# Kernel tuning notes

Hardware: AMD Instinct MI355X
Metric: run time of the kernel (lower is better)

Reference implementation:

```python
import jax, jax.numpy as jnp
import numpy as np

B = 65536
DIM = 8
HIS_LEN = 5
KIND_LEN = 10
HIS_ITEM_DIM = (1 + KIND_LEN) * DIM  # 88
ALL_DIM = DIM * (5 + KIND_LEN) + HIS_ITEM_DIM  # 208


def _linear_params(key, in_dim, out_dim):
    k1, k2 = jax.random.split(key)
    bound = 1.0 / np.sqrt(in_dim)
    w = jax.random.uniform(k1, (out_dim, in_dim), jnp.float32, -bound, bound)
    b = jax.random.uniform(k2, (out_dim,), jnp.float32, -bound, bound)
    return w, b


def setup_inputs() -> dict:
    key = jax.random.key(0)
    ks = jax.random.split(key, 20)
    inp = {
        'userid': jax.random.randint(ks[0], (B, 1), 0, 1000000),
        'itemid': jax.random.randint(ks[1], (B, 1), 0, 1000000),
        'user_age': jax.random.randint(ks[2], (B, 1), 0, 8),
        'gender': jax.random.randint(ks[3], (B, 1), 0, 3),
        'user_occupation': jax.random.randint(ks[4], (B, 1), 0, 25),
        'item_kind': jax.random.randint(ks[5], (B, KIND_LEN), 0, 20),
        'item_id_his': jax.random.randint(ks[6], (B, HIS_LEN), 0, 1000000),
        'item_kind_his': jax.random.randint(ks[7], (B, HIS_LEN, KIND_LEN), 0, 20),
        'user_emb': jax.random.normal(ks[8], (1000000, DIM), jnp.float32),
        'item_emb': jax.random.normal(ks[9], (1000000, DIM), jnp.float32),
        'age_emb': jax.random.normal(ks[10], (8, DIM), jnp.float32),
        'gender_emb': jax.random.normal(ks[11], (3, DIM), jnp.float32),
        'occ_emb': jax.random.normal(ks[12], (25, DIM), jnp.float32),
        'kind_emb': jax.random.normal(ks[13], (20, DIM), jnp.float32),
    }
    act_dims = [(HIS_ITEM_DIM * 3, 64), (64, 32), (32, 1)]
    for i, (di, do) in enumerate(act_dims, 1):
        w, b = _linear_params(jax.random.fold_in(key, 100 + i), di, do)
        inp[f'act_w{i}'], inp[f'act_b{i}'] = w, b
    mlp_dims = [(ALL_DIM, 128), (128, 64), (64, 32), (32, 1)]
    for i, (di, do) in enumerate(mlp_dims, 1):
        w, b = _linear_params(jax.random.fold_in(key, 200 + i), di, do)
        inp[f'mlp_w{i}'], inp[f'mlp_b{i}'] = w, b
    return inp


def _forward(userid, itemid, user_age, gender, user_occupation, item_kind,
             item_id_his, item_kind_his, user_emb, item_emb, age_emb,
             gender_emb, occ_emb, kind_emb,
             act_w1, act_b1, act_w2, act_b2, act_w3, act_b3,
             mlp_w1, mlp_b1, mlp_w2, mlp_b2, mlp_w3, mlp_b3, mlp_w4, mlp_b4):
    b = userid.shape[0]
    user_w = user_emb[userid]          # [b,1,8]
    item_w = item_emb[itemid]          # [b,1,8]
    age_w = age_emb[user_age]          # [b,1,8]
    gen_w = gender_emb[gender]         # [b,1,8]
    occ_w = occ_emb[user_occupation]   # [b,1,8]
    kind_w = kind_emb[item_kind]       # [b,10,8]
    kind_w = kind_w * (item_kind != 0)[..., None].astype(kind_w.dtype)

    # history: vectorized over his_len
    his_item_w = item_emb[item_id_his]           # [b,5,8]
    his_kind_w = kind_emb[item_kind_his]         # [b,5,10,8]
    his_kind_w = his_kind_w * (item_kind_his != 0)[..., None].astype(his_kind_w.dtype)
    his_feature = jnp.concatenate([his_item_w[:, :, None, :], his_kind_w], axis=2)
    his_feature = his_feature.reshape(b, HIS_LEN, HIS_ITEM_DIM)  # [b,5,88]

    item_feat_now = jnp.concatenate([item_w, kind_w], axis=1).reshape(b, 1, HIS_ITEM_DIM)
    item_feat_now = jnp.broadcast_to(item_feat_now, (b, HIS_LEN, HIS_ITEM_DIM))

    # ActUnit: i_in = [i1, i1-i2, i2]; score = MLP(i_in); act_weight = i1 * score
    i1, i2 = his_feature, item_feat_now
    i_in = jnp.concatenate([i1, i1 - i2, i2], axis=-1)  # [b,5,264]
    h = jax.nn.relu(jnp.einsum('bsd,od->bso', i_in, act_w1) + act_b1)
    h = jax.nn.relu(jnp.einsum('bsd,od->bso', h, act_w2) + act_b2)
    score = jnp.einsum('bsd,od->bso', h, act_w3) + act_b3  # [b,5,1]
    act_weight = i1 * score
    his_pool = jnp.sum(his_feature * act_weight, axis=1)  # [b,88]

    all_feat = jnp.concatenate([user_w, item_w, age_w, gen_w, occ_w, kind_w], axis=1).reshape(b, -1)
    all_feat = jnp.concatenate([all_feat, his_pool], axis=-1)  # [b,208]

    h = jax.nn.relu(all_feat @ mlp_w1.T + mlp_b1)
    h = jax.nn.relu(h @ mlp_w2.T + mlp_b2)
    h = jax.nn.relu(h @ mlp_w3.T + mlp_b3)
    logit = h @ mlp_w4.T + mlp_b4  # [b,1]
    return jax.nn.sigmoid(logit)


def reference(userid, itemid, user_age, gender, user_occupation, item_kind,
              item_id_his, item_kind_his, user_emb, item_emb, age_emb,
              gender_emb, occ_emb, kind_emb,
              act_w1, act_b1, act_w2, act_b2, act_w3, act_b3,
              mlp_w1, mlp_b1, mlp_w2, mlp_b2, mlp_w3, mlp_b3, mlp_w4, mlp_b4):
    return _forward(userid, itemid, user_age, gender, user_occupation, item_kind,
                    item_id_his, item_kind_his, user_emb, item_emb, age_emb,
                    gender_emb, occ_emb, kind_emb,
                    act_w1, act_b1, act_w2, act_b2, act_w3, act_b3,
                    mlp_w1, mlp_b1, mlp_w2, mlp_b2, mlp_w3, mlp_b3, mlp_w4, mlp_b4)
```

## Files before the change

kernel.cpp:

```cpp
#include <hip/hip_runtime.h>
#include <cstdint>
#include <math.h>

#define BATCH    65536
#define HIS_LEN  5
#define KIND_LEN 10
#define SB       64
#define NTH      256

typedef float    v2f __attribute__((ext_vector_type(2)));
typedef _Float16 v2h __attribute__((ext_vector_type(2)));
__device__ __forceinline__ v2f mk2(float a, float b){ v2f r; r.x=a; r.y=b; return r; }
#define C2H(u) __builtin_bit_cast(v2h,(unsigned)(u))

#if __has_builtin(__builtin_amdgcn_fdot2)
__device__ __forceinline__ float FD2(v2h a, v2h b, float c){
  return __builtin_amdgcn_fdot2(a, b, c, false);
}
#else
__device__ __forceinline__ float FD2(v2h a, v2h b, float c){
  return c + (float)a.x*(float)b.x + (float)a.y*(float)b.y;
}
#endif

__device__ __forceinline__ unsigned short f2h(float f){
  return __builtin_bit_cast(unsigned short, (_Float16)f);
}
__device__ __forceinline__ unsigned pack2h(float a, float b){
  return (unsigned)f2h(a) | ((unsigned)f2h(b) << 16);
}
__device__ __forceinline__ v2h pkh(float a, float b){
  return __builtin_bit_cast(v2h, __builtin_amdgcn_cvt_pkrtz(a, b));
}

#define OFF_WC1H 0
#define OFF_AB1  6144
#define OFF_W2H  6208
#define OFF_AB2  7232
#define OFF_W3   7264
#define OFF_AB3  7296
#define OFF_MB2  7297
#define OFF_MB3  7361
#define OFF_M4   7393
#define OFF_MB4  7425
#define OFF_M3H  7428
#define OFF_M1H  8452
#define OFF_MB1  22788
#define OFF_M2H  22916
#define PREP_N   27012
#define M1H4  2113
#define M2H4  5729
#define M3H4  1857

#define PFF   6144
#define W2HF4 1552
#define MBB   7426
#define TPF   7442
#define LDSF  9490

typedef const float* fp;

__device__ __forceinline__ float m1s_val(fp m1, int o, int q, int t){
  if(t >= 52) return 0.f;
  int src;
  if(t<8){ int E = (q==0)?0:(8+8*q); src = E + t; }
  else if(t<30){ int d=t-8; int idx = 8*(d>>1)+2*q+(d&1);
                 src = (idx<8) ? (8+idx) : (32+idx); }
  else { int d=t-30; int idx = 8*(d>>1)+2*q+(d&1); src = 120+idx; }
  return m1[o*208 + src];
}
__device__ __forceinline__ float w1c_val(fp aw1, int o, int q, int h, int d){
  if(d >= 22) return 0.f;
  int idx = 8*(d>>1) + 2*q + (d&1);
  return h ? (aw1[o*264+176+idx] - aw1[o*264+88+idx])
           : (aw1[o*264+idx]     + aw1[o*264+88+idx]);
}

__global__ void din_prep(fp aw1, fp ab1, fp aw2, fp ab2, fp aw3, fp ab3,
                         fp m1,  fp mb1, fp m2,  fp mb2, fp m3,  fp mb3,
                         fp m4,  fp mb4, float* __restrict__ ws){
  int j = blockIdx.x*blockDim.x + threadIdx.x;
  unsigned* wsu = (unsigned*)ws;
  if(j < 6144){
    int h = j/3072, r = j%3072;
    int slot = r/12, dw = r - slot*12;
    int o = slot>>2, q = slot&3;
    wsu[OFF_WC1H + j] = pack2h(w1c_val(aw1,o,q,h,2*dw), w1c_val(aw1,o,q,h,2*dw+1));
    return;
  } j -= 6144;
  if(j < 64){ ws[OFF_AB1 + j] = ab1[j]; return; } j -= 64;
  if(j < 1024){
    int pp = j>>5, q = (j>>3)&3, dw = j&7;
    int o = 8*q + dw;
    wsu[OFF_W2H + j] = pack2h(aw2[o*64 + 2*pp], aw2[o*64 + 2*pp+1]);
    return;
  } j -= 1024;
  if(j < 32){ ws[OFF_AB2 + j] = ab2[j]; return; } j -= 32;
  if(j < 32){ ws[OFF_W3  + j] = aw3[j]; return; } j -= 32;
  if(j < 1){ ws[OFF_AB3] = ab3[0]; return; } j -= 1;
  if(j < 64){ ws[OFF_MB2 + j] = mb2[j]; return; } j -= 64;
  if(j < 32){ ws[OFF_MB3 + j] = mb3[j]; return; } j -= 32;
  if(j < 32){ ws[OFF_M4  + j] = m4[j];  return; } j -= 32;
  if(j < 1){ ws[OFF_MB4] = mb4[0]; return; } j -= 1;
  if(j < 2){ ws[7426 + j] = 0.f; return; } j -= 2;
  if(j < 1024){
    int qq = j>>8, rr = j&255, ip = rr>>5, dw = rr&31;
    wsu[OFF_M3H + j] = pack2h(m3[dw*64 + 16*qq + 2*ip], m3[dw*64 + 16*qq + 2*ip+1]);
    return;
  } j -= 1024;
  if(j < 14336){
    int slot = j/28, dw = j - slot*28;
    int o = slot>>2, q = slot&3;
    wsu[OFF_M1H + j] = pack2h(m1s_val(m1,o,q,2*dw), m1s_val(m1,o,q,2*dw+1));
    return;
  } j -= 14336;
  if(j < 128){ ws[OFF_MB1 + j] = mb1[j]; return; } j -= 128;
  if(j < 4096){
    int gp = j>>6, q = (j>>4)&3, dw = j&15;
    int o = 16*q + dw;
    wsu[OFF_M2H + j] = pack2h(m2[o*128 + 2*gp], m2[o*128 + 2*gp+1]);
    return;
  }
}

template<int CTL>
__device__ __forceinline__ float qp(float v){
  return __uint_as_float((unsigned)__builtin_amdgcn_update_dpp(
      0, (int)__float_as_uint(v), CTL, 0xF, 0xF, true));
}
__device__ __forceinline__ float bsum4(float v){
  v += qp<0xB1>(v);
  v += qp<0x4E>(v);
  return v;
}

__device__ __forceinline__ void ldst16(void* l, const void* g){
  __builtin_amdgcn_global_load_lds(
      (const __attribute__((address_space(1))) unsigned int*)(uintptr_t)g,
      (__attribute__((address_space(3))) unsigned int*)(uintptr_t)l, 16, 0, 0);
}
__device__ __forceinline__ void ldst4(void* l, const void* g){
  __builtin_amdgcn_global_load_lds(
      (const __attribute__((address_space(1))) unsigned int*)(uintptr_t)g,
      (__attribute__((address_space(3))) unsigned int*)(uintptr_t)l, 4, 0, 0);
}

__device__ __forceinline__ void gather_h(const float2* __restrict__ itemp,
                                         const float2* __restrict__ kindp,
                                         int item_idx, const int* __restrict__ kidx,
                                         int q, v2h* f){
  float2 v = itemp[item_idx*4 + q];
  f[0] = pkh(v.x, v.y);
  #pragma unroll
  for(int r=0;r<KIND_LEN;r++){
    int ki = kidx[r];
    float2 w = kindp[ki*4 + q];
    float mx = ki ? w.x : 0.f, my = ki ? w.y : 0.f;
    f[1+r] = pkh(mx, my);
  }
}

template<int NS>
__device__ __forceinline__ void hist_pass(int b, int s0, int q, int wid,
    const float2* __restrict__ item_emb, const float2* __restrict__ kind_emb,
    const int* __restrict__ his_id, const int* __restrict__ his_kind,
    const float* ls, const float4* ls4, const unsigned* tpu, v2f* poolv){
  v2h i1h[NS][11];
  #pragma unroll
  for(int t=0;t<NS;t++)
    gather_h(item_emb, kind_emb, his_id[b*HIS_LEN + s0 + t],
             his_kind + (b*HIS_LEN + s0 + t)*KIND_LEN, q, i1h[t]);
  float h2s[NS][8];
  #pragma unroll
  for(int t=0;t<NS;t++)
    #pragma unroll
    for(int k=0;k<8;k++) h2s[t][k] = 0.f;

  #pragma unroll 1
  for(int p=0;p<32;p++){
    const uint4* wr0 = (const uint4*)(ls4 + ((2*p  )*4+q)*3);
    const uint4* wr1 = (const uint4*)(ls4 + ((2*p+1)*4+q)*3);
    uint4 r0=wr0[0], r1=wr0[1], r2=wr0[2];
    uint4 s0v=wr1[0], s1v=wr1[1], s2v=wr1[2];
    unsigned w0[12] = {r0.x,r0.y,r0.z,r0.w, r1.x,r1.y,r1.z,r1.w, r2.x,r2.y,r2.z,r2.w};
    unsigned w1[12] = {s0v.x,s0v.y,s0v.z,s0v.w, s1v.x,s1v.y,s1v.z,s1v.w, s2v.x,s2v.y,s2v.z,s2v.w};
    v2h t2 = C2H(tpu[p*SB + wid]);
    v2h hpv[NS];
    #pragma unroll
    for(int t=0;t<NS;t++){
      float aA=0.f, aB=0.f, cA=0.f, cB=0.f;
      #pragma unroll
      for(int u=0;u<11;u++){
        if(u&1){ aB = FD2(C2H(w0[u]), i1h[t][u], aB); cB = FD2(C2H(w1[u]), i1h[t][u], cB); }
        else   { aA = FD2(C2H(w0[u]), i1h[t][u], aA); cA = FD2(C2H(w1[u]), i1h[t][u], cA); }
      }
      float h0 = fmaxf(bsum4(aA+aB) + (float)t2.x, 0.f);
      float h1 = fmaxf(bsum4(cA+cB) + (float)t2.y, 0.f);
      hpv[t] = pkh(h0, h1);
    }
    uint4 wa = *(const uint4*)(ls4 + W2HF4 + (p*4+q)*2);
    uint4 wb = *(const uint4*)(ls4 + W2HF4 + (p*4+q)*2 + 1);
    unsigned w2d[8] = {wa.x,wa.y,wa.z,wa.w, wb.x,wb.y,wb.z,wb.w};
    #pragma unroll
    for(int t=0;t<NS;t++)
      #pragma unroll
      for(int k=0;k<8;k++) h2s[t][k] = FD2(C2H(w2d[k]), hpv[t], h2s[t][k]);
  }
  #pragma unroll
  for(int t=0;t<NS;t++){
    float scp = 0.f;
    #pragma unroll
    for(int j=0;j<8;j++){
      float hx = fmaxf(h2s[t][j] + ls[PFF+1088+8*q+j], 0.f);
      scp += ls[PFF+1120+8*q+j]*hx;
    }
    float sc = bsum4(scp) + ls[PFF+1152];
    #pragma unroll
    for(int j=0;j<11;j++){
      float sx = (float)i1h[t][j].x, sy = (float)i1h[t][j].y;
      poolv[j] = __builtin_elementwise_fma(mk2(sx*sc, sy*sc), mk2(sx, sy), poolv[j]);
    }
  }
}

__device__ __forceinline__ void mlp_stage(int c, int tid, float* ls, float4* ls4,
                                          const float* ws, const float4* ws4){
  int base = 768 + (c&1)*288;
  {
    const float4* src = (tid < 224) ? (ws4 + M1H4 + c*224 + tid)
                                    : (ws4 + M2H4 + c*64 + (tid-224));
    ldst16(ls4 + base + tid, src);
    if(tid < 32) ldst16(ls4 + base + 256 + tid, ws4 + M2H4 + c*64 + 32 + tid);
  }
  if(tid < 8) ldst4(ls + MBB + (c&1)*8 + tid, ws + OFF_MB1 + c*8 + tid);
}

__global__ void __launch_bounds__(NTH, 4)
din_main(const int* __restrict__ userid, const int* __restrict__ itemid,
         const int* __restrict__ age,    const int* __restrict__ gen,
         const int* __restrict__ occ,    const int* __restrict__ item_kind,
         const int* __restrict__ his_id, const int* __restrict__ his_kind,
         const float2* __restrict__ user_emb, const float2* __restrict__ item_emb,
         const float2* __restrict__ age_emb,  const float2* __restrict__ gen_emb,
         const float2* __restrict__ occ_emb,  const float2* __restrict__ kind_emb,
         const float* __restrict__ ws, float* __restrict__ out){
  const int tid  = threadIdx.x;
  const int q    = tid & 3;
  const int sl   = (tid & 63) >> 2;
  const int wv   = __builtin_amdgcn_readfirstlane(tid >> 6);
  const int wid  = wv*16 + sl;
  const int b    = blockIdx.x*SB + wid;

  __shared__ __align__(16) float ls[LDSF];
  float4* ls4 = (float4*)ls;
  const float* wsc = ws;
  const float4* ws4 = (const float4*)ws;
  unsigned* tpu = (unsigned*)(ls + TPF);

  #pragma unroll
  for(int k=0;k<5;k++){ int j = k*NTH + tid; ldst4(ls + PFF + j, wsc + OFF_AB1 + j); }
  { int j = 5*NTH + tid;
    if(j < 1282) ldst4(ls + PFF + j, wsc + OFF_AB1 + j); }
  #pragma unroll
  for(int k=0;k<6;k++){ int j = k*NTH + tid; ldst16(ls4 + j, ws4 + j); }

  v2h i2h[11];
  gather_h(item_emb, kind_emb, itemid[b], item_kind + b*KIND_LEN, q, i2h);

  __syncthreads();

  #pragma unroll 1
  for(int p=0;p<32;p++){
    const uint4* wr0 = (const uint4*)(ls4 + 768 + ((2*p  )*4+q)*3);
    const uint4* wr1 = (const uint4*)(ls4 + 768 + ((2*p+1)*4+q)*3);
    uint4 r0=wr0[0], r1=wr0[1], r2=wr0[2];
    uint4 s0v=wr1[0], s1v=wr1[1], s2v=wr1[2];
    unsigned w0[12] = {r0.x,r0.y,r0.z,r0.w, r1.x,r1.y,r1.z,r1.w, r2.x,r2.y,r2.z,r2.w};
    unsigned w1[12] = {s0v.x,s0v.y,s0v.z,s0v.w, s1v.x,s1v.y,s1v.z,s1v.w, s2v.x,s2v.y,s2v.z,s2v.w};
    float aA=0.f, aB=0.f, cA=0.f, cB=0.f;
    #pragma unroll
    for(int u=0;u<11;u++){
      if(u&1){ aB = FD2(C2H(w0[u]), i2h[u], aB); cB = FD2(C2H(w1[u]), i2h[u], cB); }
      else   { aA = FD2(C2H(w0[u]), i2h[u], aA); cA = FD2(C2H(w1[u]), i2h[u], cA); }
    }
    float sA = bsum4(aA+aB), sB = bsum4(cA+cB);
    if(q==0){
      float2 bb = ((const float2*)(ls+PFF))[p];
      tpu[p*SB + wid] = __builtin_bit_cast(unsigned, pkh(sA+bb.x, sB+bb.y));
    }
  }

  __syncthreads();

  mlp_stage(0, tid, ls, ls4, wsc, ws4);
  mlp_stage(1, tid, ls, ls4, wsc, ws4);

  v2f poolv[11];
  #pragma unroll
  for(int d=0;d<11;d++) poolv[d]=mk2(0.f,0.f);
  hist_pass<2>(b, 0, q, wid, item_emb, kind_emb, his_id, his_kind, ls, ls4, tpu, poolv);
  hist_pass<2>(b, 2, q, wid, item_emb, kind_emb, his_id, his_kind, ls, ls4, tpu, poolv);
  hist_pass<1>(b, 4, q, wid, item_emb, kind_emb, his_id, his_kind, ls, ls4, tpu, poolv);

  v2h fe[26];
  {
    const float2* ep = (q==0)? user_emb : (q==1)? age_emb : (q==2)? gen_emb : occ_emb;
    int ei = (q==0)? userid[b] : (q==1)? age[b] : (q==2)? gen[b] : occ[b];
    #pragma unroll
    for(int k=0;k<4;k++){ float2 v = ep[ei*4+k]; fe[k] = pkh(v.x, v.y); }
  }
  #pragma unroll
  for(int j=0;j<11;j++) fe[4+j]  = i2h[j];
  #pragma unroll
  for(int j=0;j<11;j++) fe[15+j] = pkh(poolv[j].x, poolv[j].y);
  float h2s2[16];
  #pragma unroll
  for(int k=0;k<16;k++) h2s2[k] = ls[PFF+1153+16*q+k];

  __syncthreads();

  #pragma unroll 1
  for(int c=0;c<16;c++){
    int base = 768 + (c&1)*288;
    #pragma unroll 1
    for(int ii=0;ii<4;ii++){
      float hh[2];
      #pragma unroll
      for(int e=0;e<2;e++){
        int i = 2*ii + e;
        const uint4* wr = (const uint4*)(ls4 + base + (i*4+q)*7);
        unsigned dwv[28];
        #pragma unroll
        for(int k=0;k<7;k++){
          uint4 t = wr[k];
          dwv[4*k]=t.x; dwv[4*k+1]=t.y; dwv[4*k+2]=t.z; dwv[4*k+3]=t.w;
        }
        float aA = 0.f, aB = 0.f;
        #pragma unroll
        for(int u=0;u<26;u++){
          if(u&1) aB = FD2(C2H(dwv[u]), fe[u], aB);
          else    aA = FD2(C2H(dwv[u]), fe[u], aA);
        }
        hh[e] = fmaxf(bsum4(aA+aB) + ls[MBB + (c&1)*8 + i], 0.f);
      }
      v2h hp = pkh(hh[0], hh[1]);
      const uint4* w2p = (const uint4*)(ls4 + base + 224 + (ii*4+q)*4);
      uint4 a0=w2p[0], a1=w2p[1], a2=w2p[2], a3=w2p[3];
      unsigned d2[16] = {a0.x,a0.y,a0.z,a0.w, a1.x,a1.y,a1.z,a1.w,
                         a2.x,a2.y,a2.z,a2.w, a3.x,a3.y,a3.z,a3.w};
      #pragma unroll
      for(int k=0;k<16;k++) h2s2[k] = FD2(C2H(d2[k]), hp, h2s2[k]);
    }
    __syncthreads();
    if(c < 14){
      mlp_stage(c+2, tid, ls, ls4, wsc, ws4);
    } else if(c == 14){
      ldst16(ls4 + (tid>>6)*66 + (tid&63), ws4 + M3H4 + tid);
    }
  }

  v2h hp3[8];
  #pragma unroll
  for(int ip=0;ip<8;ip++)
    hp3[ip] = pkh(fmaxf(h2s2[2*ip],0.f), fmaxf(h2s2[2*ip+1],0.f));

  float x = ls[PFF+1281];
  #pragma unroll
  for(int g=0;g<4;g++){
    float a[8];
    #pragma unroll
    for(int j=0;j<8;j++) a[j]=0.f;
    #pragma unroll
    for(int ip=0;ip<8;ip++){
      const uint4* w3p = (const uint4*)(ls4 + q*66 + ip*8 + 2*g);
      uint4 b0=w3p[0], b1=w3p[1];
      a[0]=FD2(C2H(b0.x),hp3[ip],a[0]); a[1]=FD2(C2H(b0.y),hp3[ip],a[1]);
      a[2]=FD2(C2H(b0.z),hp3[ip],a[2]); a[3]=FD2(C2H(b0.w),hp3[ip],a[3]);
      a[4]=FD2(C2H(b1.x),hp3[ip],a[4]); a[5]=FD2(C2H(b1.y),hp3[ip],a[5]);
      a[6]=FD2(C2H(b1.z),hp3[ip],a[6]); a[7]=FD2(C2H(b1.w),hp3[ip],a[7]);
    }
    #pragma unroll
    for(int j=0;j<8;j++) a[j] = bsum4(a[j]);
    #pragma unroll
    for(int j=0;j<8;j++)
      x += ls[PFF+1249+8*g+j] * fmaxf(a[j] + ls[PFF+1217+8*g+j], 0.f);
  }

  if(q==0) out[b] = 1.0f/(1.0f + __expf(-x));
}

extern "C" void kernel_launch(void* const* d_in, const int* in_sizes, int n_in,
                              void* d_out, int out_size, void* d_ws, size_t ws_size,
                              hipStream_t stream){
  const int* userid    = (const int*)d_in[0];
  const int* itemid    = (const int*)d_in[1];
  const int* age       = (const int*)d_in[2];
  const int* gen       = (const int*)d_in[3];
  const int* occ       = (const int*)d_in[4];
  const int* item_kind = (const int*)d_in[5];
  const int* his_id    = (const int*)d_in[6];
  const int* his_kind  = (const int*)d_in[7];
  const float2* user_emb = (const float2*)d_in[8];
  const float2* item_emb = (const float2*)d_in[9];
  const float2* age_emb  = (const float2*)d_in[10];
  const float2* gen_emb  = (const float2*)d_in[11];
  const float2* occ_emb  = (const float2*)d_in[12];
  const float2* kind_emb = (const float2*)d_in[13];
  float* ws = (float*)d_ws;

  din_prep<<<(PREP_N+255)/256, 256, 0, stream>>>(
      (fp)d_in[14], (fp)d_in[15], (fp)d_in[16], (fp)d_in[17], (fp)d_in[18], (fp)d_in[19],
      (fp)d_in[20], (fp)d_in[21], (fp)d_in[22], (fp)d_in[23], (fp)d_in[24], (fp)d_in[25],
      (fp)d_in[26], (fp)d_in[27], ws);

  din_main<<<BATCH/SB, NTH, 0, stream>>>(
      userid, itemid, age, gen, occ, item_kind, his_id, his_kind,
      user_emb, item_emb, age_emb, gen_emb, occ_emb, kind_emb,
      ws, (float*)d_out);
}
```

Measured before the change: 284.0 us.

## Run the first two MLP layers on MFMA using pre-swizzled fragment weights

Replaces the per-thread fdot2 loop over the 208->128->64 MLP layers with MFMA 16x16x32 f16 instructions. The prep kernel now writes the weights in a fragment-ordered layout. Activations are staged through LDS as A-fragments, and B-fragments are read directly from global or L2 instead of being double-buffered into LDS. This removes 16 synchronised staging iterations and the dot-product ALU work, at the cost of extra LDS transposes, more barriers and a second gather of item embeddings to save registers.

```diff
diff --git a/kernel.cpp b/kernel.cpp
--- a/kernel.cpp
+++ b/kernel.cpp
@@ -9,9 +9,12 @@
 #define NTH      256
 
 typedef float    v2f __attribute__((ext_vector_type(2)));
+typedef float    v4f __attribute__((ext_vector_type(4)));
 typedef _Float16 v2h __attribute__((ext_vector_type(2)));
+typedef _Float16 v8h __attribute__((ext_vector_type(8)));
 __device__ __forceinline__ v2f mk2(float a, float b){ v2f r; r.x=a; r.y=b; return r; }
-#define C2H(u) __builtin_bit_cast(v2h,(unsigned)(u))
+#define C2H(u)  __builtin_bit_cast(v2h,(unsigned)(u))
+#define C8H(u4) __builtin_bit_cast(v8h,(u4))
 
 #if __has_builtin(__builtin_amdgcn_fdot2)
 __device__ __forceinline__ float FD2(v2h a, v2h b, float c){
@@ -44,19 +47,21 @@
 #define OFF_M4   7393
 #define OFF_MB4  7425
 #define OFF_M3H  7428
-#define OFF_M1H  8452
+#define OFF_W1F  8452
 #define OFF_MB1  22788
-#define OFF_M2H  22916
+#define OFF_W2F  22916
 #define PREP_N   27012
-#define M1H4  2113
-#define M2H4  5729
+#define W1F4  2113
+#define W2F4  5729
 #define M3H4  1857
 
-#define PFF   6144
-#define W2HF4 1552
-#define MBB   7426
-#define TPF   7442
-#define LDSF  9490
+#define TPF   6144
+#define M3HL  1856
+#define PFF   8704
+#define W2HF4 2192
+#define MB1F  9986
+#define H2F4  1088
+#define LDSF  10114
 
 typedef const float* fp;
 
@@ -68,6 +73,9 @@
                  src = (idx<8) ? (8+idx) : (32+idx); }
   else { int d=t-30; int idx = 8*(d>>1)+2*q+(d&1); src = 120+idx; }
   return m1[o*208 + src];
+}
+__device__ __forceinline__ float m1k(fp m1, int o, int k){
+  return m1s_val(m1, o, k/56, k%56);
 }
 __device__ __forceinline__ float w1c_val(fp aw1, int o, int q, int h, int d){
   if(d >= 22) return 0.f;
@@ -109,16 +117,22 @@
     return;
   } j -= 1024;
   if(j < 14336){
-    int slot = j/28, dw = j - slot*28;
-    int o = slot>>2, q = slot&3;
-    wsu[OFF_M1H + j] = pack2h(m1s_val(m1,o,q,2*dw), m1s_val(m1,o,q,2*dw+1));
+    int frag = j>>2, jr = j&3;
+    int lane = frag & 63, nt = frag >> 6;
+    int n = nt/7, t = nt - 7*n;
+    int o = 16*n + (lane&15);
+    int k0 = t*32 + ((lane>>4)<<3) + 2*jr;
+    wsu[OFF_W1F + j] = pack2h(m1k(m1,o,k0), m1k(m1,o,k0+1));
     return;
   } j -= 14336;
   if(j < 128){ ws[OFF_MB1 + j] = mb1[j]; return; } j -= 128;
   if(j < 4096){
-    int gp = j>>6, q = (j>>4)&3, dw = j&15;
-    int o = 16*q + dw;
-    wsu[OFF_M2H + j] = pack2h(m2[o*128 + 2*gp], m2[o*128 + 2*gp+1]);
+    int frag = j>>2, jr = j&3;
+    int lane = frag & 63, nt = frag >> 6;
+    int n2 = nt>>2, t2 = nt&3;
+    int o = 16*n2 + (lane&15);
+    int k0 = t2*32 + ((lane>>4)<<3) + 2*jr;
+    wsu[OFF_W2F + j] = pack2h(m2[o*128 + k0], m2[o*128 + k0+1]);
     return;
   }
 }
@@ -221,18 +235,6 @@
       poolv[j] = __builtin_elementwise_fma(mk2(sx*sc, sy*sc), mk2(sx, sy), poolv[j]);
     }
   }
-}
-
-__device__ __forceinline__ void mlp_stage(int c, int tid, float* ls, float4* ls4,
-                                          const float* ws, const float4* ws4){
-  int base = 768 + (c&1)*288;
-  {
-    const float4* src = (tid < 224) ? (ws4 + M1H4 + c*224 + tid)
-                                    : (ws4 + M2H4 + c*64 + (tid-224));
-    ldst16(ls4 + base + tid, src);
-    if(tid < 32) ldst16(ls4 + base + 256 + tid, ws4 + M2H4 + c*64 + 32 + tid);
-  }
-  if(tid < 8) ldst4(ls + MBB + (c&1)*8 + tid, ws + OFF_MB1 + c*8 + tid);
 }
 
 __global__ void __launch_bounds__(NTH, 4)
@@ -250,17 +252,22 @@
   const int wv   = __builtin_amdgcn_readfirstlane(tid >> 6);
   const int wid  = wv*16 + sl;
   const int b    = blockIdx.x*SB + wid;
+  const int l    = tid & 63;
+  const int sA   = wv*16 + (l&15);
+  const int kb   = l >> 4;
 
   __shared__ __align__(16) float ls[LDSF];
   float4* ls4 = (float4*)ls;
   const float* wsc = ws;
   const float4* ws4 = (const float4*)ws;
+  const uint4* wsu4 = (const uint4*)ws;
   unsigned* tpu = (unsigned*)(ls + TPF);
 
   #pragma unroll
   for(int k=0;k<5;k++){ int j = k*NTH + tid; ldst4(ls + PFF + j, wsc + OFF_AB1 + j); }
   { int j = 5*NTH + tid;
     if(j < 1282) ldst4(ls + PFF + j, wsc + OFF_AB1 + j); }
+  if(tid < 128) ldst4(ls + MB1F + tid, wsc + OFF_MB1 + tid);
   #pragma unroll
   for(int k=0;k<6;k++){ int j = k*NTH + tid; ldst16(ls4 + j, ws4 + j); }
 
@@ -283,17 +290,13 @@
       if(u&1){ aB = FD2(C2H(w0[u]), i2h[u], aB); cB = FD2(C2H(w1[u]), i2h[u], cB); }
       else   { aA = FD2(C2H(w0[u]), i2h[u], aA); cA = FD2(C2H(w1[u]), i2h[u], cA); }
     }
-    float sA = bsum4(aA+aB), sB = bsum4(cA+cB);
+    float sA2 = bsum4(aA+aB), sB2 = bsum4(cA+cB);
     if(q==0){
       float2 bb = ((const float2*)(ls+PFF))[p];
-      tpu[p*SB + wid] = __builtin_bit_cast(unsigned, pkh(sA+bb.x, sB+bb.y));
-    }
-  }
-
-  __syncthreads();
-
-  mlp_stage(0, tid, ls, ls4, wsc, ws4);
-  mlp_stage(1, tid, ls, ls4, wsc, ws4);
+      tpu[p*SB + wid] = __builtin_bit_cast(unsigned, pkh(sA2+bb.x, sB2+bb.y));
+    }
+  }
+  __syncthreads();
 
   v2f poolv[11];
   #pragma unroll
@@ -302,6 +305,7 @@
   hist_pass<2>(b, 2, q, wid, item_emb, kind_emb, his_id, his_kind, ls, ls4, tpu, poolv);
   hist_pass<1>(b, 4, q, wid, item_emb, kind_emb, his_id, his_kind, ls, ls4, tpu, poolv);
 
+  gather_h(item_emb, kind_emb, itemid[b], item_kind + b*KIND_LEN, q, i2h);
   v2h fe[26];
   {
     const float2* ep = (q==0)? user_emb : (q==1)? age_emb : (q==2)? gen_emb : occ_emb;
@@ -313,57 +317,88 @@
   for(int j=0;j<11;j++) fe[4+j]  = i2h[j];
   #pragma unroll
   for(int j=0;j<11;j++) fe[15+j] = pkh(poolv[j].x, poolv[j].y);
-  float h2s2[16];
-  #pragma unroll
-  for(int k=0;k<16;k++) h2s2[k] = ls[PFF+1153+16*q+k];
-
-  __syncthreads();
-
-  #pragma unroll 1
-  for(int c=0;c<16;c++){
-    int base = 768 + (c&1)*288;
-    #pragma unroll 1
-    for(int ii=0;ii<4;ii++){
-      float hh[2];
+
+  __syncthreads();
+
+  {
+    unsigned xd[28];
+    #pragma unroll
+    for(int u=0;u<26;u++) xd[u] = __builtin_bit_cast(unsigned, fe[u]);
+    xd[26] = 0; xd[27] = 0;
+    uint4* xp = (uint4*)(ls4 + wid*29 + q*7);
+    #pragma unroll
+    for(int ct=0; ct<7; ct++){
+      uint4 t; t.x=xd[4*ct]; t.y=xd[4*ct+1]; t.z=xd[4*ct+2]; t.w=xd[4*ct+3];
+      xp[ct] = t;
+    }
+  }
+  __syncthreads();
+
+  uint4 af[7];
+  #pragma unroll
+  for(int t=0;t<7;t++) af[t] = *(const uint4*)(ls4 + sA*29 + t*4 + kb);
+
+  ldst16(ls4 + M3HL + (tid>>6)*66 + (tid&63), ws4 + M3H4 + tid);
+
+  __syncthreads();
+
+  v4f acc1[8];
+  #pragma unroll
+  for(int n=0;n<8;n++){
+    float bb = ls[MB1F + n*16 + (l&15)];
+    v4f c = {bb, bb, bb, bb};
+    #pragma unroll
+    for(int t=0;t<7;t++){
+      uint4 bw = wsu4[W1F4 + (n*7+t)*64 + l];
+      c = __builtin_amdgcn_mfma_f32_16x16x32_f16(C8H(af[t]), C8H(bw), c, 0, 0, 0);
+    }
+    acc1[n] = c;
+  }
+  {
+    _Float16* h1p = (_Float16*)ls;
+    #pragma unroll
+    for(int n=0;n<8;n++)
       #pragma unroll
-      for(int e=0;e<2;e++){
-        int i = 2*ii + e;
-        const uint4* wr = (const uint4*)(ls4 + base + (i*4+q)*7);
-        unsigned dwv[28];
-        #pragma unroll
-        for(int k=0;k<7;k++){
-          uint4 t = wr[k];
-          dwv[4*k]=t.x; dwv[4*k+1]=t.y; dwv[4*k+2]=t.z; dwv[4*k+3]=t.w;
-        }
-        float aA = 0.f, aB = 0.f;
-        #pragma unroll
-        for(int u=0;u<26;u++){
-          if(u&1) aB = FD2(C2H(dwv[u]), fe[u], aB);
-          else    aA = FD2(C2H(dwv[u]), fe[u], aA);
-        }
-        hh[e] = fmaxf(bsum4(aA+aB) + ls[MBB + (c&1)*8 + i], 0.f);
-      }
-      v2h hp = pkh(hh[0], hh[1]);
-      const uint4* w2p = (const uint4*)(ls4 + base + 224 + (ii*4+q)*4);
-      uint4 a0=w2p[0], a1=w2p[1], a2=w2p[2], a3=w2p[3];
-      unsigned d2[16] = {a0.x,a0.y,a0.z,a0.w, a1.x,a1.y,a1.z,a1.w,
-                         a2.x,a2.y,a2.z,a2.w, a3.x,a3.y,a3.z,a3.w};
+      for(int i=0;i<4;i++)
+        h1p[(wv*16 + kb*4 + i)*136 + 16*n + (l&15)] =
+            (_Float16)fmaxf(acc1[n][i], 0.f);
+  }
+  __syncthreads();
+
+  v4f acc2[4];
+  #pragma unroll
+  for(int n2=0;n2<4;n2++){
+    float bb = ls[PFF+1153 + n2*16 + (l&15)];
+    v4f c = {bb, bb, bb, bb};
+    acc2[n2] = c;
+  }
+  #pragma unroll
+  for(int t2=0;t2<4;t2++){
+    uint4 aw = *(const uint4*)(ls4 + sA*17 + t2*4 + kb);
+    #pragma unroll
+    for(int n2=0;n2<4;n2++){
+      uint4 bw = wsu4[W2F4 + (n2*4+t2)*64 + l];
+      acc2[n2] = __builtin_amdgcn_mfma_f32_16x16x32_f16(C8H(aw), C8H(bw), acc2[n2], 0, 0, 0);
+    }
+  }
+  {
+    _Float16* h2p = (_Float16*)(ls4 + H2F4);
+    #pragma unroll
+    for(int n2=0;n2<4;n2++)
       #pragma unroll
-      for(int k=0;k<16;k++) h2s2[k] = FD2(C2H(d2[k]), hp, h2s2[k]);
-    }
-    __syncthreads();
-    if(c < 14){
-      mlp_stage(c+2, tid, ls, ls4, wsc, ws4);
-    } else if(c == 14){
-      ldst16(ls4 + (tid>>6)*66 + (tid&63), ws4 + M3H4 + tid);
-    }
-  }
+      for(int i=0;i<4;i++)
+        h2p[(wv*16 + kb*4 + i)*72 + 16*n2 + (l&15)] =
+            (_Float16)fmaxf(acc2[n2][i], 0.f);
+  }
+  __syncthreads();
 
   v2h hp3[8];
-  #pragma unroll
-  for(int ip=0;ip<8;ip++)
-    hp3[ip] = pkh(fmaxf(h2s2[2*ip],0.f), fmaxf(h2s2[2*ip+1],0.f));
-
+  {
+    const uint4* hr = (const uint4*)(ls4 + H2F4 + wid*9 + 2*q);
+    uint4 d0 = hr[0], d1 = hr[1];
+    hp3[0]=C2H(d0.x); hp3[1]=C2H(d0.y); hp3[2]=C2H(d0.z); hp3[3]=C2H(d0.w);
+    hp3[4]=C2H(d1.x); hp3[5]=C2H(d1.y); hp3[6]=C2H(d1.z); hp3[7]=C2H(d1.w);
+  }
   float x = ls[PFF+1281];
   #pragma unroll
   for(int g=0;g<4;g++){
@@ -372,7 +407,7 @@
     for(int j=0;j<8;j++) a[j]=0.f;
     #pragma unroll
     for(int ip=0;ip<8;ip++){
-      const uint4* w3p = (const uint4*)(ls4 + q*66 + ip*8 + 2*g);
+      const uint4* w3p = (const uint4*)(ls4 + M3HL + q*66 + ip*8 + 2*g);
       uint4 b0=w3p[0], b1=w3p[1];
       a[0]=FD2(C2H(b0.x),hp3[ip],a[0]); a[1]=FD2(C2H(b0.y),hp3[ip],a[1]);
       a[2]=FD2(C2H(b0.z),hp3[ip],a[2]); a[3]=FD2(C2H(b0.w),hp3[ip],a[3]);
```

After: 242.2 us. -14.7%, faster.
